# Kernel tuning notes

Hardware: AMD Instinct MI355X
Metric: run time of the kernel (lower is better)

The kernel has to match this reference:

```python
import jax, jax.numpy as jnp
import numpy as np

B_PAIR = 8      # batch_size (identities)
NUM_POS = 4     # images per identity
TEMP = 50.0     # softmax temperature
DIM = 2048
H, W = 24, 12
HALF = B_PAIR * NUM_POS  # 32 samples per modality


def _rand_pairs(rng):
    # mirrors CMAlign._random_pairs
    pos = np.concatenate([rng.permutation(NUM_POS) + NUM_POS * i for i in range(B_PAIR)])
    neg = []
    for i in range(B_PAIR):
        others = np.array([j for j in range(B_PAIR) if j != i])
        bidx = rng.choice(others, NUM_POS, replace=False)
        nidx = rng.permutation(NUM_POS)
        neg.append(bidx * NUM_POS + nidx)
    return pos.astype(np.int32), np.concatenate(neg).astype(np.int32)


def setup_inputs() -> dict:
    key = jax.random.key(0)
    ks = jax.random.split(key, 8)
    feat_v = jax.random.normal(ks[0], (HALF, DIM, H, W), jnp.float32)
    feat_t = jax.random.normal(ks[1], (HALF, DIM, H, W), jnp.float32)
    uncertain_v = jax.random.normal(ks[2], (HALF, 1, H, W), jnp.float32)
    uncertain_t = jax.random.normal(ks[3], (HALF, 1, H, W), jnp.float32)
    q_w = jax.random.normal(ks[4], (DIM // 4, DIM, 3, 3), jnp.float32) * 0.02
    q_b = jnp.zeros((DIM // 4,), jnp.float32)
    k_w = jax.random.normal(ks[5], (DIM // 4, DIM, 3, 3), jnp.float32) * 0.02
    k_b = jnp.zeros((DIM // 4,), jnp.float32)
    rng = np.random.RandomState(0)
    pos_v, neg_v = _rand_pairs(rng)
    pos_t, neg_t = _rand_pairs(rng)
    # visible queries target thermal half (offset), thermal queries target visible half
    pos_idx = jnp.asarray(np.concatenate([pos_v + HALF, pos_t]), jnp.int32)
    neg_idx = jnp.asarray(np.concatenate([neg_v + HALF, neg_t]), jnp.int32)
    return dict(feat_v=feat_v, feat_t=feat_t, uncertain_v=uncertain_v,
                uncertain_t=uncertain_t, q_w=q_w, q_b=q_b, k_w=k_w, k_b=k_b,
                pos_idx=pos_idx, neg_idx=neg_idx)


def _conv3x3(x, w, b):
    y = jax.lax.conv_general_dilated(x, w, window_strides=(1, 1),
                                     padding=((1, 1), (1, 1)),
                                     dimension_numbers=('NCHW', 'OIHW', 'NCHW'))
    return y + b[None, :, None, None]


def _l2n(x, axis):
    # torch F.normalize: x / max(||x||, 1e-12)
    n = jnp.sqrt(jnp.sum(x * x, axis=axis, keepdims=True))
    return x / jnp.maximum(n, 1e-12)


def _cmalign(feat_v, feat_t, q_w, q_b, k_w, k_b, pos_idx, neg_idx):
    feat = jnp.concatenate([feat_v, feat_t], axis=0)  # [B,C,h,w]
    B, C, h, w = feat.shape
    HW = h * w

    # compute_mask (detached): per-sample min-max normalized channel L2 norm
    norms = jnp.sqrt(jnp.sum(feat * feat, axis=1)).reshape(B, HW)
    norms = norms - jnp.min(norms, axis=-1, keepdims=True)
    norms = norms / (jnp.max(norms, axis=-1, keepdims=True) + 1e-12)
    mask = jax.lax.stop_gradient(norms.reshape(B, 1, h, w))

    fq = _conv3x3(feat, q_w, q_b).reshape(B, C // 4, HW)  # query proj shared

    def matching_pr(target):
        fk = _conv3x3(target, k_w, k_b).reshape(B, C // 4, HW)
        sim = jnp.einsum('bcq,bck->bqk', _l2n(fq, 1), _l2n(fk, 1))
        # max-subtract + exp + sum == stable softmax with temperature
        return jax.nn.softmax(TEMP * sim, axis=-1)

    def warp_recon(pr, target):
        warp = jnp.einsum('bqk,bck->bcq', pr, target.reshape(B, C, HW)).reshape(B, C, h, w)
        return mask * warp + (1.0 - mask) * feat

    # positive branch
    tgt_pos = feat[pos_idx]
    pr_pos = matching_pr(tgt_pos)
    mq = mask.reshape(B, HW, 1)
    mk = mask[pos_idx].reshape(B, HW, 1)
    comask = (mq * jnp.einsum('bqk,bko->bqo', pr_pos, mk)).reshape(B, HW)
    comask = comask - jnp.min(comask, axis=-1, keepdims=True)
    comask = comask / (jnp.max(comask, axis=-1, keepdims=True) + 1e-12)
    comask = jax.lax.stop_gradient(comask.reshape(B, h, w))
    feat_recon_pos = warp_recon(pr_pos, tgt_pos)

    # negative branch
    tgt_neg = feat[neg_idx]
    feat_recon_neg = warp_recon(matching_pr(tgt_neg), tgt_neg)

    # triplet margin loss (p=2, margin=0.3, eps=1e-6), distance over channel dim
    d_ap = jnp.sqrt(jnp.sum((feat - feat_recon_pos + 1e-6) ** 2, axis=1))  # [B,h,w]
    d_an = jnp.sqrt(jnp.sum((feat - feat_recon_neg + 1e-6) ** 2, axis=1))
    trip = jnp.maximum(d_ap - d_an + 0.3, 0.0)
    loss = jnp.mean(comask * trip)
    return feat_recon_pos, loss


def reference(feat_v, feat_t, uncertain_v, uncertain_t, q_w, q_b, k_w, k_b, pos_idx, neg_idx):
    # uncertain_v/uncertain_t are concatenated but unused in CMAlign.forward (faithful)
    del uncertain_v, uncertain_t
    return _cmalign(feat_v, feat_t, q_w, q_b, k_w, k_b, pos_idx, neg_idx)
```

## Files before the change

kernel.cpp:

```cpp
#include <hip/hip_runtime.h>
#include <cstdint>
#include <cstddef>


namespace {
constexpr int kB    = 64;
constexpr int kHalf = 32;
constexpr int kC    = 2048;
constexpr int kCQ   = 512;
constexpr int kH    = 24;
constexpr int kW    = 12;
constexpr int kHW   = 288;
constexpr float kTemp = 50.0f;
constexpr int kXPlane = 366;
}

typedef __attribute__((ext_vector_type(8))) __bf16 bf16x8;
typedef __attribute__((ext_vector_type(4))) float f32x4;
typedef __attribute__((ext_vector_type(8))) unsigned short ushort8;

__device__ __forceinline__ const float* feat_base(const float* fv, const float* ft, int b) {
  return (b < kHalf) ? (fv + (size_t)b * kC * kHW)
                     : (ft + (size_t)(b - kHalf) * kC * kHW);
}

__device__ __forceinline__ unsigned short f2bf(float f) {
  union { float f; unsigned u; } c; c.f = f;
  unsigned u = c.u;
  unsigned r = (u + 0x7FFFu + ((u >> 16) & 1u)) >> 16;
  return (unsigned short)r;
}

__device__ __forceinline__ float bf2f(unsigned short h) {
  union { unsigned u; float f; } c; c.u = ((unsigned)h) << 16;
  return c.f;
}

__device__ __forceinline__ void gload_lds16(const void* g, void* l) {
  __builtin_amdgcn_global_load_lds(
      (const __attribute__((address_space(1))) unsigned int*)g,
      (__attribute__((address_space(3))) unsigned int*)l, 16, 0, 0);
}

__global__ void zero_kernel(float* __restrict__ p, int n) {
  int i = blockIdx.x * 256 + threadIdx.x;
  if (i < n) p[i] = 0.f;
}

__global__ __launch_bounds__(256) void prep_w_kernel(const float* __restrict__ qw,
                                                     const float* __restrict__ kw,
                                                     unsigned short* __restrict__ wtq,
                                                     unsigned short* __restrict__ wtk) {
  int oc = blockIdx.x;
  int z  = blockIdx.y;
  const float* w = (z ? kw : qw) + (size_t)oc * (kC * 9);
  unsigned short* wt = z ? wtk : wtq;
  __shared__ unsigned short lw[kC * 9];
  int t = threadIdx.x;
#pragma unroll
  for (int it = 0; it < 18; ++it) {
    int i4 = (it * 256 + t) * 4;
    float4 v = *(const float4*)(w + i4);
    lw[i4 + 0] = f2bf(v.x);
    lw[i4 + 1] = f2bf(v.y);
    lw[i4 + 2] = f2bf(v.z);
    lw[i4 + 3] = f2bf(v.w);
  }
  __syncthreads();
  for (int item = t; item < 9 * 256; item += 256) {
    int tap = item >> 8;
    int icb = item & 255;
    ushort8 pk;
#pragma unroll
    for (int j = 0; j < 8; ++j) pk[j] = lw[(icb * 8 + j) * 9 + tap];
    size_t dst16 = (((size_t)(icb >> 2) * 9 + tap) * 32 + (oc >> 4)) * 64
                   + (oc & 15) + (icb & 3) * 16;
    *(ushort8*)(wt + dst16 * 8) = pk;
  }
}

__global__ __launch_bounds__(512, 1) void conv_fused_kernel(const unsigned short* __restrict__ wtq,
                                                            const unsigned short* __restrict__ wtk,
                                                            const float* __restrict__ qb,
                                                            const float* __restrict__ kb,
                                                            const float* __restrict__ fv,
                                                            const float* __restrict__ ft,
                                                            unsigned short* __restrict__ fqT,
                                                            unsigned short* __restrict__ fkT,
                                                            float* __restrict__ qss,
                                                            float* __restrict__ kss,
                                                            float* __restrict__ maskb) {
  __shared__ unsigned short Wbuf[2 * 6 * 4096];
  __shared__ unsigned short Xs[4 * kXPlane * 8];
  int t    = threadIdx.x;
  int lane = t & 63;
  int wid  = t >> 6;
  int l15  = lane & 15, kg = lane >> 4;
  int wm   = wid & 1, wn = wid >> 1;
  int n    = blockIdx.x;
  int xcd  = n & 7;
  int oc0  = (xcd >> 1) * 128;
  int b    = ((xcd & 1) << 5) + (n >> 3);
  int f0   = oc0 >> 4;
  const float* fb = feat_base(fv, ft, b);
  const char* wtqB = (const char*)wtq;
  const char* wtkB = (const char*)wtk;

  int  xoff[3];
  bool xvalid[3], xhas[3];
#pragma unroll
  for (int i = 0; i < 3; ++i) {
    int item = i * 512 + t;
    xhas[i] = item < 4 * kXPlane;
    int xkg = item / kXPlane;
    int hp  = item - xkg * kXPlane;
    int hy = hp / 14, hx = hp - hy * 14;
    int y = hy - 1, x = hx - 1;
    bool v = xhas[i] && hp < 364 && (y >= 0 && y < kH && x >= 0 && x < kW);
    xvalid[i] = v;
    xoff[i] = v ? (xkg * 8) * kHW + y * kW + x : 0;
  }

  int aAddr[4];
#pragma unroll
  for (int fm = 0; fm < 4; ++fm)
    aAddr[fm] = (((wm * 4 + fm) * 64) + lane) * 16;
  int nfn = (wn < 2) ? 5 : 4;
  int fnb = (wn < 2) ? wn * 5 : 10 + (wn - 2) * 4;
  int bAddr[5];
#pragma unroll
  for (int fi = 0; fi < 5; ++fi) {
    int p = (fnb + fi) * 16 + l15;
    if (p > 287) p = 287;
    int y = p / kW, x = p - y * kW;
    bAddr[fi] = kg * (kXPlane * 16) + ((y + 1) * 14 + (x + 1)) * 16;
  }

  f32x4 acc[2][4][5];
#pragma unroll
  for (int cv = 0; cv < 2; ++cv)
#pragma unroll
    for (int fm = 0; fm < 4; ++fm)
#pragma unroll
      for (int fi = 0; fi < 5; ++fi) acc[cv][fm][fi] = (f32x4){0.f, 0.f, 0.f, 0.f};

  float msum0 = 0.f, msum1 = 0.f, msum2 = 0.f;

  char* WsB = (char*)Wbuf;
  char* XsB = (char*)Xs;
  int wavebase = t & ~63;

#pragma unroll
  for (int i = 0; i < 3; ++i) {
    if (xhas[i] && !xvalid[i]) {
      ushort8 pk;
#pragma unroll
      for (int j = 0; j < 8; ++j) pk[j] = 0;
      *(ushort8*)(XsB + (size_t)(i * 512 + t) * 16) = pk;
    }
  }
#pragma unroll
  for (int r = 0; r < 3; ++r) {
    size_t g16 = ((size_t)r * 32 + f0 + wid) * 64 + lane;
    gload_lds16(wtqB + g16 * 16, WsB + (size_t)(r * 2 + 0) * 8192 + wavebase * 16);
    gload_lds16(wtkB + g16 * 16, WsB + (size_t)(r * 2 + 1) * 8192 + wavebase * 16);
  }

  int buf = 0;
#pragma unroll 1
  for (int chunk = 0; chunk < 64; ++chunk) {
    int ic0 = chunk * 32;
    {
      float xv[3][8];
#pragma unroll
      for (int i = 0; i < 3; ++i)
        if (xvalid[i]) {
          const float* s = fb + (size_t)ic0 * kHW + xoff[i];
#pragma unroll
          for (int j = 0; j < 8; ++j) xv[i][j] = s[(size_t)j * kHW];
        }
      if (xvalid[0]) {
#pragma unroll
        for (int j = 0; j < 8; ++j) msum0 = fmaf(xv[0][j], xv[0][j], msum0);
      }
      if (xvalid[1]) {
#pragma unroll
        for (int j = 0; j < 8; ++j) msum1 = fmaf(xv[1][j], xv[1][j], msum1);
      }
      if (xvalid[2]) {
#pragma unroll
        for (int j = 0; j < 8; ++j) msum2 = fmaf(xv[2][j], xv[2][j], msum2);
      }
#pragma unroll
      for (int i = 0; i < 3; ++i) {
        if (!xvalid[i]) continue;
        ushort8 pk;
#pragma unroll
        for (int j = 0; j < 8; ++j) pk[j] = f2bf(xv[i][j]);
        *(ushort8*)(XsB + (size_t)(i * 512 + t) * 16) = pk;
      }
    }
    __syncthreads();

#pragma unroll 1
    for (int g = 0; g < 3; ++g) {
      bool hn = (g < 2) || (chunk < 63);
      if (hn) {
        int nchunk = (g < 2) ? chunk : chunk + 1;
        int ng     = (g < 2) ? g + 1 : 0;
#pragma unroll
        for (int r = 0; r < 3; ++r) {
          size_t g16 = ((size_t)(nchunk * 9 + ng * 3 + r) * 32 + f0 + wid) * 64 + lane;
          gload_lds16(wtqB + g16 * 16,
                      WsB + (size_t)((buf ^ 1) * 6 + r * 2 + 0) * 8192 + wavebase * 16);
          gload_lds16(wtkB + g16 * 16,
                      WsB + (size_t)((buf ^ 1) * 6 + r * 2 + 1) * 8192 + wavebase * 16);
        }
      }
#pragma unroll
      for (int r = 0; r < 3; ++r) {
        int tap = g * 3 + r;
        int d16 = ((tap / 3 - 1) * 14 + (tap % 3 - 1)) * 16;
        bf16x8 af[2][4];
#pragma unroll
        for (int cv = 0; cv < 2; ++cv)
#pragma unroll
          for (int fm = 0; fm < 4; ++fm)
            af[cv][fm] = *(const bf16x8*)(WsB + (size_t)(buf * 6 + r * 2 + cv) * 8192 + aAddr[fm]);
#pragma unroll
        for (int fi = 0; fi < 5; ++fi) {
          if (fi >= nfn) continue;
          bf16x8 bb = *(const bf16x8*)(XsB + bAddr[fi] + d16);
#pragma unroll
          for (int cv = 0; cv < 2; ++cv)
#pragma unroll
            for (int fm = 0; fm < 4; ++fm)
              acc[cv][fm][fi] =
                  __builtin_amdgcn_mfma_f32_16x16x32_bf16(af[cv][fm], bb, acc[cv][fm][fi], 0, 0, 0);
        }
      }
      __syncthreads();
      buf ^= 1;
    }
  }

  if (oc0 == 0) {
    float* Mred = (float*)Xs;
    float msum[3] = {msum0, msum1, msum2};
#pragma unroll
    for (int i = 0; i < 3; ++i) {
      if (!xvalid[i]) continue;
      int item = i * 512 + t;
      int xkg = item / kXPlane;
      int hp  = item - xkg * kXPlane;
      int y = hp / 14 - 1, x = hp % 14 - 1;
      Mred[xkg * kHW + y * kW + x] = msum[i];
    }
    __syncthreads();
    float nv = 0.f;
    if (t < kHW)
      nv = sqrtf(Mred[t] + Mred[kHW + t] + Mred[2 * kHW + t] + Mred[3 * kHW + t]);
    float* red = (float*)Wbuf;
    red[t] = (t < kHW) ? nv : 3.4e38f;
    __syncthreads();
    float mn;
    {
      float m = 3.4e38f;
      if (t < 64) {
        for (int i = t; i < 512; i += 64) m = fminf(m, red[i]);
        for (int off = 32; off; off >>= 1) m = fminf(m, __shfl_xor(m, off));
      }
      __syncthreads();
      if (t == 0) red[0] = m;
      __syncthreads();
      mn = red[0];
      __syncthreads();
    }
    red[t] = (t < kHW) ? nv : -3.4e38f;
    __syncthreads();
    float mx;
    {
      float m = -3.4e38f;
      if (t < 64) {
        for (int i = t; i < 512; i += 64) m = fmaxf(m, red[i]);
        for (int off = 32; off; off >>= 1) m = fmaxf(m, __shfl_xor(m, off));
      }
      __syncthreads();
      if (t == 0) red[0] = m;
      __syncthreads();
      mx = red[0];
    }
    if (t < kHW) maskb[b * kHW + t] = (nv - mn) / ((mx - mn) + 1e-12f);
    __syncthreads();
  }

  unsigned short* Ep = Wbuf;
#pragma unroll
  for (int cv = 0; cv < 2; ++cv) {
    const float* bias = cv ? kb : qb;
    float* ssq = cv ? kss : qss;
#pragma unroll
    for (int fi = 0; fi < 5; ++fi) {
      if (fi >= nfn) continue;
      int p = (fnb + fi) * 16 + l15;
      float ps = 0.f;
#pragma unroll
      for (int fm = 0; fm < 4; ++fm)
#pragma unroll
        for (int reg = 0; reg < 4; ++reg) {
          int ocl = wm * 64 + fm * 16 + kg * 4 + reg;
          float v = acc[cv][fm][fi][reg] + bias[oc0 + ocl];
          ps = fmaf(v, v, ps);
          Ep[p * 136 + ocl] = f2bf(v);
        }
      ps += __shfl_xor(ps, 16);
      ps += __shfl_xor(ps, 32);
      if (kg == 0) atomicAdd(ssq + b * kHW + p, ps);
    }
    __syncthreads();
    unsigned short* dstT = (cv ? fkT : fqT) + (size_t)b * kHW * kCQ + oc0;
#pragma unroll
    for (int it = 0; it < 9; ++it) {
      int item = it * 512 + t;
      int p = item >> 4, j = item & 15;
      *(ushort8*)(dstT + (size_t)p * kCQ + j * 8) =
          *(const ushort8*)(Ep + p * 136 + j * 8);
    }
    __syncthreads();
  }
}

__global__ __launch_bounds__(512) void warp_mfma_kernel(const float* __restrict__ fv,
                                                        const float* __restrict__ ft,
                                                        const unsigned short* __restrict__ prb0,
                                                        const unsigned short* __restrict__ prb1,
                                                        const float* __restrict__ maskp,
                                                        const int* __restrict__ pos_idx,
                                                        const int* __restrict__ neg_idx,
                                                        float* __restrict__ outp,
                                                        float* __restrict__ dap,
                                                        float* __restrict__ dan) {
  __shared__ unsigned short AsHi[128 * 32];
  __shared__ unsigned short AsLo[128 * 32];
  __shared__ unsigned short Bs[288 * 32];
  int t    = threadIdx.x;
  int lane = t & 63;
  int wid  = t >> 6;
  int l15  = lane & 15, kg = lane >> 4;
  int wm   = wid >> 1, wn = wid & 1;
  int n    = blockIdx.x;
  int xcd  = n & 7;
  int m    = n >> 3;
  int b    = xcd + ((m & 7) << 3);
  int rest = m >> 3;
  int c0   = (rest & 15) * 128;
  int z    = rest >> 4;
  int write_out = (z == 0);
  const unsigned short* prb = z ? prb1 : prb0;
  float* dsq = z ? dan : dap;
  int tb   = (z ? neg_idx : pos_idx)[b];
  const float* tgt = feat_base(fv, ft, tb);
  const float* fb  = feat_base(fv, ft, b);

  int ar = t >> 2, as = t & 3;
  int aslot = as ^ ((ar ^ (ar >> 2)) & 3);
  unsigned short* aDstHi = AsHi + ar * 32 + aslot * 8;
  unsigned short* aDstLo = AsLo + ar * 32 + aslot * 8;

  int aIdx[2];
#pragma unroll
  for (int fm = 0; fm < 2; ++fm) {
    int r = wm * 32 + fm * 16 + l15;
    aIdx[fm] = r * 32 + (kg ^ ((r ^ (r >> 2)) & 3)) * 8;
  }
  int bIdx[9];
#pragma unroll
  for (int fn = 0; fn < 9; ++fn) {
    int q = wn * 144 + fn * 16 + l15;
    bIdx[fn] = q * 32 + (kg ^ ((q ^ (q >> 2)) & 3)) * 8;
  }

  f32x4 acc[2][9];
#pragma unroll
  for (int fm = 0; fm < 2; ++fm)
#pragma unroll
    for (int fn = 0; fn < 9; ++fn) acc[fm][fn] = (f32x4){0.f, 0.f, 0.f, 0.f};

#pragma unroll 1
  for (int chunk = 0; chunk < 9; ++chunk) {
    int k0 = chunk * 32;
    __syncthreads();
    {
      const float* s = tgt + (size_t)(c0 + ar) * kHW + k0 + as * 8;
      float4 v0 = *(const float4*)(s);
      float4 v1 = *(const float4*)(s + 4);
      float xs[8] = {v0.x, v0.y, v0.z, v0.w, v1.x, v1.y, v1.z, v1.w};
      ushort8 hi, lo;
#pragma unroll
      for (int j = 0; j < 8; ++j) {
        unsigned short h = f2bf(xs[j]);
        hi[j] = h;
        lo[j] = f2bf(xs[j] - bf2f(h));
      }
      *(ushort8*)aDstHi = hi;
      *(ushort8*)aDstLo = lo;
    }
#pragma unroll
    for (int i = 0; i < 3; ++i) {
      int item = i * 512 + t;
      if (item < 1152) {
        int q = item >> 2, s = item & 3;
        ushort8 v = *(const ushort8*)(prb + ((size_t)b * kHW + q) * kHW + k0 + s * 8);
        *(ushort8*)(Bs + q * 32 + (s ^ ((q ^ (q >> 2)) & 3)) * 8) = v;
      }
    }
    __syncthreads();
    bf16x8 ah0 = *(const bf16x8*)(AsHi + aIdx[0]);
    bf16x8 al0 = *(const bf16x8*)(AsLo + aIdx[0]);
    bf16x8 ah1 = *(const bf16x8*)(AsHi + aIdx[1]);
    bf16x8 al1 = *(const bf16x8*)(AsLo + aIdx[1]);
#pragma unroll
    for (int fn = 0; fn < 9; ++fn) {
      bf16x8 bb = *(const bf16x8*)(Bs + bIdx[fn]);
      acc[0][fn] = __builtin_amdgcn_mfma_f32_16x16x32_bf16(ah0, bb, acc[0][fn], 0, 0, 0);
      acc[0][fn] = __builtin_amdgcn_mfma_f32_16x16x32_bf16(al0, bb, acc[0][fn], 0, 0, 0);
      acc[1][fn] = __builtin_amdgcn_mfma_f32_16x16x32_bf16(ah1, bb, acc[1][fn], 0, 0, 0);
      acc[1][fn] = __builtin_amdgcn_mfma_f32_16x16x32_bf16(al1, bb, acc[1][fn], 0, 0, 0);
    }
  }

#pragma unroll
  for (int fn = 0; fn < 9; ++fn) {
    int q = wn * 144 + fn * 16 + l15;
    float mj = maskp[b * kHW + q];
    float psum = 0.f;
#pragma unroll
    for (int fm = 0; fm < 2; ++fm) {
#pragma unroll
      for (int reg = 0; reg < 4; ++reg) {
        int c = c0 + wm * 32 + fm * 16 + kg * 4 + reg;
        float fvv = fb[(size_t)c * kHW + q];
        float Wv  = acc[fm][fn][reg];
        float d   = mj * (fvv - Wv) + 1e-6f;
        psum      = fmaf(d, d, psum);
        if (write_out)
          outp[((size_t)b * kC + c) * kHW + q] = mj * Wv + (1.f - mj) * fvv;
      }
    }
    psum += __shfl_xor(psum, 16);
    psum += __shfl_xor(psum, 32);
    if (lane < 16) atomicAdd(&dsq[b * kHW + q], psum);
  }
}

__global__ __launch_bounds__(512, 1) void sim_mfma_kernel(const unsigned short* __restrict__ fqT,
                                                          const unsigned short* __restrict__ fkT,
                                                          const float* __restrict__ qss,
                                                          const float* __restrict__ kss,
                                                          const float* __restrict__ maskb,
                                                          const int* __restrict__ pos_idx,
                                                          const int* __restrict__ neg_idx,
                                                          unsigned short* __restrict__ prb0,
                                                          unsigned short* __restrict__ prb1,
                                                          float* __restrict__ craw) {
  __shared__ float Sbuf[96 * 289];
  __shared__ float mtl[kHW];
  unsigned short* As = (unsigned short*)Sbuf;
  unsigned short* Bs = (unsigned short*)((char*)Sbuf + 6144);
  float (*S)[289] = (float(*)[289])Sbuf;
  int t    = threadIdx.x;
  int lane = t & 63;
  int wid  = t >> 6;
  int l15  = lane & 15, kg = lane >> 4;
  int wm   = wid & 1, wn = wid >> 1;
  int n    = blockIdx.x;
  int xcd  = n & 7;
  int m    = n >> 3;
  int b    = xcd + ((m & 7) << 3);
  int rest = m >> 3;
  int q0   = (rest % 3) * 96;
  int z    = rest / 3;
  int tb   = (z ? neg_idx : pos_idx)[b];
  unsigned short* prb = z ? prb1 : prb0;
  const unsigned short* fqb = fqT + ((size_t)b * kHW + q0) * kCQ;
  const unsigned short* fkb = fkT + (size_t)tb * kHW * kCQ;

  if (t < kHW) mtl[t] = maskb[tb * kHW + t];

  int aIdx[3];
#pragma unroll
  for (int fm = 0; fm < 3; ++fm) {
    int r = wm * 48 + fm * 16 + l15;
    aIdx[fm] = r * 32 + (kg ^ ((r ^ (r >> 2)) & 3)) * 8;
  }
  int nfn = (wn < 2) ? 5 : 4;
  int fnb = (wn < 2) ? wn * 5 : 10 + (wn - 2) * 4;
  int bIdx[5];
#pragma unroll
  for (int fi = 0; fi < 5; ++fi) {
    int kr = (fnb + fi) * 16 + l15;
    if (kr > 287) kr = 287;
    bIdx[fi] = kr * 32 + (kg ^ ((kr ^ (kr >> 2)) & 3)) * 8;
  }

  f32x4 acc[3][5];
#pragma unroll
  for (int fm = 0; fm < 3; ++fm)
#pragma unroll
    for (int fi = 0; fi < 5; ++fi) acc[fm][fi] = (f32x4){0.f, 0.f, 0.f, 0.f};

#pragma unroll 1
  for (int chunk = 0; chunk < 16; ++chunk) {
    int c0 = chunk * 32;
    __syncthreads();
    if (t < 384) {
      int ar = t >> 2, as = t & 3;
      ushort8 v = *(const ushort8*)(fqb + (size_t)ar * kCQ + c0 + as * 8);
      int slot = as ^ ((ar ^ (ar >> 2)) & 3);
      *(ushort8*)(As + ar * 32 + slot * 8) = v;
    }
#pragma unroll
    for (int i = 0; i < 3; ++i) {
      int item = i * 512 + t;
      if (item < 1152) {
        int kr = item >> 2, ks = item & 3;
        ushort8 v = *(const ushort8*)(fkb + (size_t)kr * kCQ + c0 + ks * 8);
        int slot = ks ^ ((kr ^ (kr >> 2)) & 3);
        *(ushort8*)(Bs + kr * 32 + slot * 8) = v;
      }
    }
    __syncthreads();
    bf16x8 a[3];
#pragma unroll
    for (int fm = 0; fm < 3; ++fm) a[fm] = *(const bf16x8*)(As + aIdx[fm]);
#pragma unroll
    for (int fi = 0; fi < 5; ++fi) {
      if (fi >= nfn) continue;
      bf16x8 bb = *(const bf16x8*)(Bs + bIdx[fi]);
#pragma unroll
      for (int fm = 0; fm < 3; ++fm)
        acc[fm][fi] = __builtin_amdgcn_mfma_f32_16x16x32_bf16(a[fm], bb, acc[fm][fi], 0, 0, 0);
    }
  }
  __syncthreads();

  float kinvv[5];
#pragma unroll
  for (int fi = 0; fi < 5; ++fi) {
    int col = (fnb + fi) * 16 + l15;
    if (col > 287) col = 287;
    kinvv[fi] = 1.f / fmaxf(sqrtf(kss[tb * kHW + col]), 1e-12f);
  }
#pragma unroll
  for (int fm = 0; fm < 3; ++fm)
#pragma unroll
    for (int reg = 0; reg < 4; ++reg) {
      int row = wm * 48 + fm * 16 + kg * 4 + reg;
      float qi = kTemp / fmaxf(sqrtf(qss[b * kHW + q0 + row]), 1e-12f);
#pragma unroll
      for (int fi = 0; fi < 5; ++fi) {
        if (fi >= nfn) continue;
        S[row][(fnb + fi) * 16 + l15] = qi * kinvv[fi] * acc[fm][fi][reg];
      }
    }
  __syncthreads();

  int l = lane;
  for (int q = wid; q < 96; q += 8) {
    float v[5];
    float m2 = -3.4e38f;
#pragma unroll
    for (int j = 0; j < 5; ++j) {
      int k = l + 64 * j;
      v[j] = (k < kHW) ? S[q][k] : -3.4e38f;
      m2 = fmaxf(m2, v[j]);
    }
    for (int off = 32; off; off >>= 1) m2 = fmaxf(m2, __shfl_xor(m2, off));
    float e[5];
    float s = 0.f;
#pragma unroll
    for (int j = 0; j < 5; ++j) {
      int k = l + 64 * j;
      e[j] = (k < kHW) ? __expf(v[j] - m2) : 0.f;
      s += e[j];
    }
    for (int off = 32; off; off >>= 1) s += __shfl_xor(s, off);
    float invs = 1.f / s;
    unsigned short* row = prb + ((size_t)b * kHW + q0 + q) * kHW;
    float dot = 0.f;
#pragma unroll
    for (int j = 0; j < 5; ++j) {
      int k = l + 64 * j;
      if (k < kHW) {
        float p = e[j] * invs;
        row[k] = f2bf(p);
        if (z == 0) dot = fmaf(bf2f(f2bf(p)), mtl[k], dot);
      }
    }
    if (z == 0) {
      for (int off = 32; off; off >>= 1) dot += __shfl_xor(dot, off);
      if (l == 0)
        craw[b * kHW + q0 + q] = maskb[b * kHW + q0 + q] * dot;
    }
  }
}

__global__ __launch_bounds__(256) void loss_kernel(const float* __restrict__ dap,
                                                   const float* __restrict__ dan,
                                                   const float* __restrict__ craw,
                                                   float* __restrict__ out) {
  int t = threadIdx.x;
  int wv = t >> 6, l = t & 63;
  __shared__ float sh4a[4], sh4b[4];
  __shared__ float sh2[2];
  float total = 0.f;
#pragma unroll 1
  for (int b = 0; b < kB; ++b) {
    const float* cb = craw + b * kHW;
    float v1 = cb[t];
    float v2 = (t < kHW - 256) ? cb[t + 256] : v1;
    float mnl = fminf(v1, v2), mxl = fmaxf(v1, v2);
    for (int off = 32; off; off >>= 1) {
      mnl = fminf(mnl, __shfl_xor(mnl, off));
      mxl = fmaxf(mxl, __shfl_xor(mxl, off));
    }
    if (l == 0) { sh4a[wv] = mnl; sh4b[wv] = mxl; }
    __syncthreads();
    if (t == 0) {
      float mn = sh4a[0], mx = sh4b[0];
      for (int i = 1; i < 4; ++i) { mn = fminf(mn, sh4a[i]); mx = fmaxf(mx, sh4b[i]); }
      sh2[0] = mn; sh2[1] = mx;
    }
    __syncthreads();
    float mn = sh2[0];
    float inv = 1.f / ((sh2[1] - mn) + 1e-12f);
    {
      int i = b * kHW + t;
      float cn = (v1 - mn) * inv;
      float tr = fmaxf(sqrtf(dap[i]) - sqrtf(dan[i]) + 0.3f, 0.f);
      total = fmaf(cn, tr, total);
    }
    if (t < kHW - 256) {
      int i = b * kHW + t + 256;
      float cn = (v2 - mn) * inv;
      float tr = fmaxf(sqrtf(dap[i]) - sqrtf(dan[i]) + 0.3f, 0.f);
      total = fmaf(cn, tr, total);
    }
    __syncthreads();
  }
  for (int off = 32; off; off >>= 1) total += __shfl_xor(total, off);
  if (l == 0) sh4a[wv] = total;
  __syncthreads();
  if (t == 0)
    out[(size_t)kB * kC * kHW] =
        (sh4a[0] + sh4a[1] + sh4a[2] + sh4a[3]) * (1.f / (float)(kB * kHW));
}

extern "C" void kernel_launch(void* const* d_in, const int* in_sizes, int n_in,
                              void* d_out, int out_size, void* d_ws, size_t ws_size,
                              hipStream_t stream) {
  const float* fv = (const float*)d_in[0];
  const float* ft = (const float*)d_in[1];
  const float* qw = (const float*)d_in[4];
  const float* qb = (const float*)d_in[5];
  const float* kw = (const float*)d_in[6];
  const float* kb = (const float*)d_in[7];
  const int* pos_idx = (const int*)d_in[8];
  const int* neg_idx = (const int*)d_in[9];
  float* out = (float*)d_out;

  constexpr size_t kFQ = (size_t)kB * kCQ * kHW;
  constexpr size_t kPR = (size_t)kB * kHW * kHW;
  float* ws   = (float*)d_ws;
  unsigned short* fqT = (unsigned short*)ws;
  unsigned short* fkT = fqT + (size_t)kB * kHW * kCQ;
  unsigned short* prb0 = (unsigned short*)(ws + kFQ);
  unsigned short* prb1 = prb0 + kPR;
  unsigned short* wtq = (unsigned short*)(ws + 2 * kFQ);
  unsigned short* wtk = wtq + (size_t)9 * kCQ * kC;
  float* maskb   = (float*)(wtk + (size_t)9 * kCQ * kC);
  float* qss     = maskb + kB * kHW;
  float* kss     = qss + kB * kHW;
  float* craw    = kss + kB * kHW;
  float* dap     = craw + kB * kHW;
  float* dan     = dap + kB * kHW;
  if (ws_size < (size_t)113688576) return;

  zero_kernel<<<dim3((5 * kB * kHW + 255) / 256), 256, 0, stream>>>(qss, 5 * kB * kHW);
  prep_w_kernel<<<dim3(kCQ, 2), 256, 0, stream>>>(qw, kw, wtq, wtk);
  conv_fused_kernel<<<dim3(256), 512, 0, stream>>>(wtq, wtk, qb, kb, fv, ft,
                                                   fqT, fkT, qss, kss, maskb);
  sim_mfma_kernel<<<dim3(384), 512, 0, stream>>>(fqT, fkT, qss, kss, maskb,
                                                 pos_idx, neg_idx, prb0, prb1, craw);
  warp_mfma_kernel<<<dim3(2048), 512, 0, stream>>>(fv, ft, prb0, prb1, maskb,
                                                   pos_idx, neg_idx, out, dap, dan);
  loss_kernel<<<dim3(1), 256, 0, stream>>>(dap, dan, craw, out);
}
```

Measured before the change: 1.040 ms.

## Halve conv output-channel tile to run two blocks per CU

Each conv block now computes 64 output channels for both Q and K convolutions instead of 128. The grid doubles to 512 blocks, remapped so batch index varies across XCDs. The weight LDS buffer, accumulators and epilogue staging shrink, and launch bounds allow more resident blocks so latency can be hidden by co-resident blocks. In exchange, each input feature tile is loaded, squared and converted to bf16 by twice as many blocks, and reuse of each B fragment across MFMAs is halved.

```diff
diff --git a/kernel.cpp b/kernel.cpp
--- a/kernel.cpp
+++ b/kernel.cpp
@@ -79,7 +79,7 @@
   }
 }
 
-__global__ __launch_bounds__(512, 1) void conv_fused_kernel(const unsigned short* __restrict__ wtq,
+__global__ __launch_bounds__(512, 4) void conv_fused_kernel(const unsigned short* __restrict__ wtq,
                                                             const unsigned short* __restrict__ wtk,
                                                             const float* __restrict__ qb,
                                                             const float* __restrict__ kb,
@@ -90,18 +90,20 @@
                                                             float* __restrict__ qss,
                                                             float* __restrict__ kss,
                                                             float* __restrict__ maskb) {
-  __shared__ unsigned short Wbuf[2 * 6 * 4096];
+  __shared__ unsigned short Wbuf[2 * 6 * 2048];
   __shared__ unsigned short Xs[4 * kXPlane * 8];
   int t    = threadIdx.x;
   int lane = t & 63;
+  int l15  = lane & 15, kg = lane >> 4;
   int wid  = t >> 6;
-  int l15  = lane & 15, kg = lane >> 4;
   int wm   = wid & 1, wn = wid >> 1;
   int n    = blockIdx.x;
   int xcd  = n & 7;
-  int oc0  = (xcd >> 1) * 128;
-  int b    = ((xcd & 1) << 5) + (n >> 3);
-  int f0   = oc0 >> 4;
+  int idx  = n >> 3;
+  int b    = xcd + ((idx & 7) << 3);
+  int mt   = idx >> 3;
+  int oc0  = mt * 64;
+  int f0   = mt * 4;
   const float* fb = feat_base(fv, ft, b);
   const char* wtqB = (const char*)wtq;
   const char* wtkB = (const char*)wtk;
@@ -121,10 +123,10 @@
     xoff[i] = v ? (xkg * 8) * kHW + y * kW + x : 0;
   }
 
-  int aAddr[4];
-#pragma unroll
-  for (int fm = 0; fm < 4; ++fm)
-    aAddr[fm] = (((wm * 4 + fm) * 64) + lane) * 16;
+  int aAddr[2];
+#pragma unroll
+  for (int fm = 0; fm < 2; ++fm)
+    aAddr[fm] = (((wm * 2 + fm) * 64) + lane) * 16;
   int nfn = (wn < 2) ? 5 : 4;
   int fnb = (wn < 2) ? wn * 5 : 10 + (wn - 2) * 4;
   int bAddr[5];
@@ -136,11 +138,11 @@
     bAddr[fi] = kg * (kXPlane * 16) + ((y + 1) * 14 + (x + 1)) * 16;
   }
 
-  f32x4 acc[2][4][5];
+  f32x4 acc[2][2][5];
 #pragma unroll
   for (int cv = 0; cv < 2; ++cv)
 #pragma unroll
-    for (int fm = 0; fm < 4; ++fm)
+    for (int fm = 0; fm < 2; ++fm)
 #pragma unroll
       for (int fi = 0; fi < 5; ++fi) acc[cv][fm][fi] = (f32x4){0.f, 0.f, 0.f, 0.f};
 
@@ -160,45 +162,49 @@
     }
   }
 #pragma unroll
-  for (int r = 0; r < 3; ++r) {
-    size_t g16 = ((size_t)r * 32 + f0 + wid) * 64 + lane;
-    gload_lds16(wtqB + g16 * 16, WsB + (size_t)(r * 2 + 0) * 8192 + wavebase * 16);
-    gload_lds16(wtkB + g16 * 16, WsB + (size_t)(r * 2 + 1) * 8192 + wavebase * 16);
+  for (int k = 0; k < 3; ++k) {
+    int i  = k * 512 + t;
+    int s  = i >> 8;
+    int cv = s & 1, rr = s >> 1;
+    int frag = (i >> 6) & 3;
+    const char* wsrc = cv ? wtkB : wtqB;
+    size_t g16 = ((size_t)rr * 32 + f0 + frag) * 64 + lane;
+    gload_lds16(wsrc + g16 * 16, WsB + (size_t)(k * 512 + wavebase) * 16);
   }
 
   int buf = 0;
 #pragma unroll 1
   for (int chunk = 0; chunk < 64; ++chunk) {
     int ic0 = chunk * 32;
-    {
-      float xv[3][8];
-#pragma unroll
-      for (int i = 0; i < 3; ++i)
-        if (xvalid[i]) {
-          const float* s = fb + (size_t)ic0 * kHW + xoff[i];
-#pragma unroll
-          for (int j = 0; j < 8; ++j) xv[i][j] = s[(size_t)j * kHW];
-        }
-      if (xvalid[0]) {
-#pragma unroll
-        for (int j = 0; j < 8; ++j) msum0 = fmaf(xv[0][j], xv[0][j], msum0);
-      }
-      if (xvalid[1]) {
-#pragma unroll
-        for (int j = 0; j < 8; ++j) msum1 = fmaf(xv[1][j], xv[1][j], msum1);
-      }
-      if (xvalid[2]) {
-#pragma unroll
-        for (int j = 0; j < 8; ++j) msum2 = fmaf(xv[2][j], xv[2][j], msum2);
-      }
-#pragma unroll
-      for (int i = 0; i < 3; ++i) {
-        if (!xvalid[i]) continue;
-        ushort8 pk;
-#pragma unroll
-        for (int j = 0; j < 8; ++j) pk[j] = f2bf(xv[i][j]);
-        *(ushort8*)(XsB + (size_t)(i * 512 + t) * 16) = pk;
-      }
+    if (xvalid[0]) {
+      const float* s = fb + (size_t)ic0 * kHW + xoff[0];
+      float xv[8];
+#pragma unroll
+      for (int j = 0; j < 8; ++j) xv[j] = s[(size_t)j * kHW];
+      ushort8 pk;
+#pragma unroll
+      for (int j = 0; j < 8; ++j) { msum0 = fmaf(xv[j], xv[j], msum0); pk[j] = f2bf(xv[j]); }
+      *(ushort8*)(XsB + (size_t)t * 16) = pk;
+    }
+    if (xvalid[1]) {
+      const float* s = fb + (size_t)ic0 * kHW + xoff[1];
+      float xv[8];
+#pragma unroll
+      for (int j = 0; j < 8; ++j) xv[j] = s[(size_t)j * kHW];
+      ushort8 pk;
+#pragma unroll
+      for (int j = 0; j < 8; ++j) { msum1 = fmaf(xv[j], xv[j], msum1); pk[j] = f2bf(xv[j]); }
+      *(ushort8*)(XsB + (size_t)(512 + t) * 16) = pk;
+    }
+    if (xvalid[2]) {
+      const float* s = fb + (size_t)ic0 * kHW + xoff[2];
+      float xv[8];
+#pragma unroll
+      for (int j = 0; j < 8; ++j) xv[j] = s[(size_t)j * kHW];
+      ushort8 pk;
+#pragma unroll
+      for (int j = 0; j < 8; ++j) { msum2 = fmaf(xv[j], xv[j], msum2); pk[j] = f2bf(xv[j]); }
+      *(ushort8*)(XsB + (size_t)(1024 + t) * 16) = pk;
     }
     __syncthreads();
 
@@ -209,24 +215,28 @@
         int nchunk = (g < 2) ? chunk : chunk + 1;
         int ng     = (g < 2) ? g + 1 : 0;
 #pragma unroll
-        for (int r = 0; r < 3; ++r) {
-          size_t g16 = ((size_t)(nchunk * 9 + ng * 3 + r) * 32 + f0 + wid) * 64 + lane;
-          gload_lds16(wtqB + g16 * 16,
-                      WsB + (size_t)((buf ^ 1) * 6 + r * 2 + 0) * 8192 + wavebase * 16);
-          gload_lds16(wtkB + g16 * 16,
-                      WsB + (size_t)((buf ^ 1) * 6 + r * 2 + 1) * 8192 + wavebase * 16);
+        for (int k = 0; k < 3; ++k) {
+          int i  = k * 512 + t;
+          int s  = i >> 8;
+          int cv = s & 1, rr = s >> 1;
+          int frag = (i >> 6) & 3;
+          const char* wsrc = cv ? wtkB : wtqB;
+          size_t g16 = ((size_t)(nchunk * 9 + ng * 3 + rr) * 32 + f0 + frag) * 64 + lane;
+          gload_lds16(wsrc + g16 * 16,
+                      WsB + (size_t)((buf ^ 1) * 1536 + k * 512 + wavebase) * 16);
         }
       }
 #pragma unroll
       for (int r = 0; r < 3; ++r) {
         int tap = g * 3 + r;
         int d16 = ((tap / 3 - 1) * 14 + (tap % 3 - 1)) * 16;
-        bf16x8 af[2][4];
+        bf16x8 af[2][2];
 #pragma unroll
         for (int cv = 0; cv < 2; ++cv)
 #pragma unroll
-          for (int fm = 0; fm < 4; ++fm)
-            af[cv][fm] = *(const bf16x8*)(WsB + (size_t)(buf * 6 + r * 2 + cv) * 8192 + aAddr[fm]);
+          for (int fm = 0; fm < 2; ++fm)
+            af[cv][fm] =
+                *(const bf16x8*)(WsB + (size_t)(buf * 6 + r * 2 + cv) * 4096 + aAddr[fm]);
 #pragma unroll
         for (int fi = 0; fi < 5; ++fi) {
           if (fi >= nfn) continue;
@@ -234,7 +244,7 @@
 #pragma unroll
           for (int cv = 0; cv < 2; ++cv)
 #pragma unroll
-            for (int fm = 0; fm < 4; ++fm)
+            for (int fm = 0; fm < 2; ++fm)
               acc[cv][fm][fi] =
                   __builtin_amdgcn_mfma_f32_16x16x32_bf16(af[cv][fm], bb, acc[cv][fm][fi], 0, 0, 0);
         }
@@ -244,7 +254,7 @@
     }
   }
 
-  if (oc0 == 0) {
+  if (mt == 0) {
     float* Mred = (float*)Xs;
     float msum[3] = {msum0, msum1, msum2};
 #pragma unroll
@@ -305,13 +315,13 @@
       int p = (fnb + fi) * 16 + l15;
       float ps = 0.f;
 #pragma unroll
-      for (int fm = 0; fm < 4; ++fm)
+      for (int fm = 0; fm < 2; ++fm)
 #pragma unroll
         for (int reg = 0; reg < 4; ++reg) {
-          int ocl = wm * 64 + fm * 16 + kg * 4 + reg;
+          int ocl = wm * 32 + fm * 16 + kg * 4 + reg;
           float v = acc[cv][fm][fi][reg] + bias[oc0 + ocl];
           ps = fmaf(v, v, ps);
-          Ep[p * 136 + ocl] = f2bf(v);
+          Ep[p * 72 + ocl] = f2bf(v);
         }
       ps += __shfl_xor(ps, 16);
       ps += __shfl_xor(ps, 32);
@@ -320,11 +330,13 @@
     __syncthreads();
     unsigned short* dstT = (cv ? fkT : fqT) + (size_t)b * kHW * kCQ + oc0;
 #pragma unroll
-    for (int it = 0; it < 9; ++it) {
+    for (int it = 0; it < 5; ++it) {
       int item = it * 512 + t;
-      int p = item >> 4, j = item & 15;
-      *(ushort8*)(dstT + (size_t)p * kCQ + j * 8) =
-          *(const ushort8*)(Ep + p * 136 + j * 8);
+      if (item < 2304) {
+        int p = item >> 3, j = item & 7;
+        *(ushort8*)(dstT + (size_t)p * kCQ + j * 8) =
+            *(const ushort8*)(Ep + p * 72 + j * 8);
+      }
     }
     __syncthreads();
   }
@@ -688,7 +700,7 @@
 
   zero_kernel<<<dim3((5 * kB * kHW + 255) / 256), 256, 0, stream>>>(qss, 5 * kB * kHW);
   prep_w_kernel<<<dim3(kCQ, 2), 256, 0, stream>>>(qw, kw, wtq, wtk);
-  conv_fused_kernel<<<dim3(256), 512, 0, stream>>>(wtq, wtk, qb, kb, fv, ft,
+  conv_fused_kernel<<<dim3(512), 512, 0, stream>>>(wtq, wtk, qb, kb, fv, ft,
                                                    fqT, fkT, qss, kss, maskb);
   sim_mfma_kernel<<<dim3(384), 512, 0, stream>>>(fqT, fkT, qss, kss, maskb,
                                                  pos_idx, neg_idx, prb0, prb1, craw);
```

Result: faster. 1.006 ms (-3.3%).
